# Kernel tuning notes

Hardware: AMD Instinct MI355X
Metric: run time of the kernel (lower is better)

Reference implementation:

```python
import jax, jax.numpy as jnp
import numpy as np

B, N, H = 8, 2048, 256


def setup_inputs() -> dict:
    key = jax.random.key(0)
    ks = jax.random.split(key, 8)
    s = 1.0 / np.sqrt(H)
    return {
        "node": jax.random.normal(ks[0], (B, N, H), dtype=jnp.float32),
        "graph": jax.random.uniform(ks[1], (B, N, N), dtype=jnp.float32),
        "W1": jax.random.normal(ks[2], (H, H), dtype=jnp.float32) * s,
        "b1": jnp.zeros((H,), dtype=jnp.float32),
        "W2": jax.random.normal(ks[3], (H, H), dtype=jnp.float32) * s,
        "b2": jnp.zeros((H,), dtype=jnp.float32),
        "Wout": jax.random.normal(ks[4], (H, 2 * H), dtype=jnp.float32) * (1.0 / np.sqrt(2 * H)),
        "bout": jnp.zeros((H,), dtype=jnp.float32),
    }


def reference(node, graph, W1, b1, W2, b2, Wout, bout):
    # Symmetric normalization D^{-1/2} A D^{-1/2}, batched and vectorized
    # (equivalent to the per-sample diag-mm loop in the original).
    d = jnp.sum(graph, axis=2)                # [B, N] row sums (torch sum(1) on [N,N])
    dinv = d ** -0.5                          # [B, N]
    g = graph * dinv[:, :, None] * dinv[:, None, :]  # [B, N, N]

    # node_info = relu(fc1(g @ node)); fc2(g @ node_info)
    h = jax.nn.relu(jnp.einsum("bnm,bmh->bnh", g, node) @ W1.T + b1)
    h = jax.nn.relu(jnp.einsum("bnm,bmh->bnh", g, h) @ W2.T + b2)

    agg = jnp.concatenate([node, h], axis=2)  # [B, N, 2H]
    return jax.nn.relu(agg @ Wout.T + bout)   # [B, N, H]
```

## Files before the change

### kernel.cpp

```cpp
#include <hip/hip_runtime.h>
#include <stdint.h>

typedef __attribute__((ext_vector_type(4))) float f32x4;
typedef __attribute__((ext_vector_type(8))) short bf16x8;

static __device__ __forceinline__ unsigned short f2bf(float x) {
  unsigned int u = __builtin_bit_cast(unsigned int, x);
  u = (u + 0x7fffu + ((u >> 16) & 1u)) >> 16;
  return (unsigned short)u;
}

#define GLD16(g, l)                                                            \
  __builtin_amdgcn_global_load_lds(                                            \
      (__attribute__((address_space(1))) const void*)(g),                      \
      (__attribute__((address_space(3))) void*)(l), 16, 0, 0)

__global__ __launch_bounds__(256) void rowscale_cvt_k(
    const float* __restrict__ g, float* __restrict__ dinv,
    unsigned short* __restrict__ gb) {
  int row = blockIdx.x * 4 + (threadIdx.x >> 6);
  int lane = threadIdx.x & 63;
  const float* p = g + (long)row * 2048;
  float4 v[8];
  float s = 0.f;
#pragma unroll
  for (int i = 0; i < 8; ++i) {
    v[i] = *(const float4*)(p + (lane + i * 64) * 4);
    s += v[i].x + v[i].y + v[i].z + v[i].w;
  }
#pragma unroll
  for (int off = 32; off; off >>= 1) s += __shfl_xor(s, off, 64);
  float di = rsqrtf(s);
  if (lane == 0) dinv[row] = di;
  unsigned short* q = gb + (long)row * 2048;
#pragma unroll
  for (int i = 0; i < 8; ++i) {
    ushort4 u;
    u.x = f2bf(v[i].x * di); u.y = f2bf(v[i].y * di);
    u.z = f2bf(v[i].z * di); u.w = f2bf(v[i].w * di);
    *(ushort4*)(q + (lane + i * 64) * 4) = u;
  }
}

__global__ __launch_bounds__(256) void cvt_w_k(const float* __restrict__ W1,
                                               const float* __restrict__ W2,
                                               const float* __restrict__ Wout,
                                               unsigned short* __restrict__ wb) {
  int idx = blockIdx.x * 256 + threadIdx.x;
  float v;
  if (idx < 65536) v = W1[idx];
  else if (idx < 131072) v = W2[idx - 65536];
  else v = Wout[idx - 131072];
  wb[idx] = f2bf(v);
}

__global__ __launch_bounds__(256) void prep_node_k(
    const float* __restrict__ node, const float* __restrict__ dinv,
    unsigned short* __restrict__ nodeT, unsigned short* __restrict__ agg) {
  __shared__ unsigned short t[64 * 68];
  int tid = threadIdx.x;
  int m0 = blockIdx.x * 64, h0 = blockIdx.y * 64;
  long b = blockIdx.z;
#pragma unroll
  for (int i = 0; i < 4; ++i) {
    int idx = tid + 256 * i;
    int r = idx >> 4, c4 = idx & 15;
    long m = m0 + r;
    float4 v = *(const float4*)(node + (b * 2048 + m) * 256 + h0 + c4 * 4);
    float di = dinv[b * 2048 + m];
    ushort4 u;
    u.x = f2bf(v.x); u.y = f2bf(v.y); u.z = f2bf(v.z); u.w = f2bf(v.w);
    *(ushort4*)(agg + (b * 2048 + m) * 512 + h0 + c4 * 4) = u;
    t[(c4 * 4 + 0) * 68 + r] = f2bf(v.x * di);
    t[(c4 * 4 + 1) * 68 + r] = f2bf(v.y * di);
    t[(c4 * 4 + 2) * 68 + r] = f2bf(v.z * di);
    t[(c4 * 4 + 3) * 68 + r] = f2bf(v.w * di);
  }
  __syncthreads();
#pragma unroll
  for (int i = 0; i < 4; ++i) {
    int idx = tid + 256 * i;
    int hr = idx >> 4, c4 = idx & 15;
    ushort4 o = *(const ushort4*)(&t[hr * 68 + c4 * 4]);
    *(ushort4*)(nodeT + (b * 256 + h0 + hr) * 2048 + m0 + c4 * 4) = o;
  }
}

template <bool BIAS, bool RELU, bool SCALE, bool TRANS, bool OUTF32>
__global__ __launch_bounds__(256) void gemm32(
    const unsigned short* __restrict__ A, const unsigned short* __restrict__ Bt,
    const float* __restrict__ bias, const float* __restrict__ scale,
    void* __restrict__ Cp, int K, int lda, int ldbt, long bBatch, int ldc) {
  __shared__ char lds[73728];
  char* ldsA = lds;
  char* ldsB = lds + 8192;

  int tid = threadIdx.x;
  int lane = tid & 63;
  int w = tid >> 6;

  int bid = blockIdx.x;
  int tile = ((bid & 7) << 6) + (bid >> 3);
  int row0 = tile * 32;
  int batch = row0 >> 11;
  const unsigned short* Bb = Bt + (long)batch * bBatch;

  int nt = K >> 6;
  f32x4 acc[2][4] = {};

  auto stageA = [&](int kt, int buf) {
    int slot = w * 64 + lane;
    int r = slot >> 3, j = slot & 7;
    int jg = j ^ (r & 7);
    GLD16(A + (long)(row0 + r) * lda + kt * 64 + jg * 8,
          ldsA + buf * 4096 + w * 1024);
  };
  auto stageB = [&](int kt, int buf) {
    char* base = ldsB + buf * 32768;
#pragma unroll
    for (int i = 0; i < 8; ++i) {
      int slot = (w * 8 + i) * 64 + lane;
      int c = slot >> 3, j = slot & 7;
      int jg = j ^ (c & 7);
      GLD16(Bb + (long)c * ldbt + kt * 64 + jg * 8, base + (w * 8 + i) * 1024);
    }
  };
  auto compute = [&](int buf) {
    char* bA = ldsA + buf * 4096;
    char* bB = ldsB + buf * 32768;
    bf16x8 a[2][2], bb[4][2];
#pragma unroll
    for (int m = 0; m < 2; ++m)
#pragma unroll
      for (int kk = 0; kk < 2; ++kk) {
        int row = m * 16 + (lane & 15);
        int off = (row * 128 + kk * 64 + (lane >> 4) * 16) ^ ((row & 7) << 4);
        a[m][kk] = *(const bf16x8*)(bA + off);
      }
#pragma unroll
    for (int n = 0; n < 4; ++n)
#pragma unroll
      for (int kk = 0; kk < 2; ++kk) {
        int col = w * 64 + n * 16 + (lane & 15);
        int off = (col * 128 + kk * 64 + (lane >> 4) * 16) ^ ((col & 7) << 4);
        bb[n][kk] = *(const bf16x8*)(bB + off);
      }
#pragma unroll
    for (int m = 0; m < 2; ++m)
#pragma unroll
      for (int n = 0; n < 4; ++n) {
        acc[m][n] = __builtin_amdgcn_mfma_f32_16x16x32_bf16(a[m][0], bb[n][0],
                                                            acc[m][n], 0, 0, 0);
        acc[m][n] = __builtin_amdgcn_mfma_f32_16x16x32_bf16(a[m][1], bb[n][1],
                                                            acc[m][n], 0, 0, 0);
      }
  };

  stageA(0, 0);
  stageB(0, 0);
  __syncthreads();

  int cur = 0;
  for (int t = 0; t < nt; ++t) {
    int nxt = cur ^ 1;
    if (t + 1 < nt) {
      stageA(t + 1, nxt);
      stageB(t + 1, nxt);
    }
    compute(cur);
    __syncthreads();
    cur = nxt;
  }

  if (TRANS) {
    unsigned short* tb = (unsigned short*)lds;
#pragma unroll
    for (int m = 0; m < 2; ++m)
#pragma unroll
      for (int n = 0; n < 4; ++n) {
        int col = w * 64 + n * 16 + (lane & 15);
        float bv = BIAS ? bias[col] : 0.f;
#pragma unroll
        for (int r = 0; r < 4; ++r) {
          int rl = m * 16 + (lane >> 4) * 4 + r;
          float v = acc[m][n][r];
          if (BIAS) v += bv;
          if (RELU) v = fmaxf(v, 0.f);
          if (SCALE) v *= scale[row0 + rl];
          tb[col * 40 + rl] = f2bf(v);
        }
      }
    __syncthreads();
    unsigned short* C = (unsigned short*)Cp;
    int rin = row0 & 2047;
#pragma unroll
    for (int cc = 0; cc < 4; ++cc) {
      int col = (tid >> 2) + cc * 64;
      int seg = tid & 3;
      bf16x8 u = *(const bf16x8*)(tb + col * 40 + seg * 8);
      *(bf16x8*)(C + ((long)batch * 256 + col) * 2048 + rin + seg * 8) = u;
    }
  } else {
#pragma unroll
    for (int m = 0; m < 2; ++m)
#pragma unroll
      for (int n = 0; n < 4; ++n) {
        int col = w * 64 + n * 16 + (lane & 15);
        float bv = BIAS ? bias[col] : 0.f;
#pragma unroll
        for (int r = 0; r < 4; ++r) {
          long row = row0 + m * 16 + (lane >> 4) * 4 + r;
          float v = acc[m][n][r];
          if (BIAS) v += bv;
          if (RELU) v = fmaxf(v, 0.f);
          if (SCALE) v *= scale[row];
          if (OUTF32) ((float*)Cp)[row * ldc + col] = v;
          else ((unsigned short*)Cp)[row * ldc + col] = f2bf(v);
        }
      }
  }
}

extern "C" void kernel_launch(void* const* d_in, const int* in_sizes, int n_in,
                              void* d_out, int out_size, void* d_ws,
                              size_t ws_size, hipStream_t stream) {
  const float* node = (const float*)d_in[0];
  const float* graph = (const float*)d_in[1];
  const float* W1 = (const float*)d_in[2];
  const float* b1 = (const float*)d_in[3];
  const float* W2 = (const float*)d_in[4];
  const float* b2 = (const float*)d_in[5];
  const float* Wout = (const float*)d_in[6];
  const float* bout = (const float*)d_in[7];
  float* out = (float*)d_out;

  char* p = (char*)d_ws;
  float* dinv = (float*)p;                    p += 16384 * 4;
  unsigned short* wb = (unsigned short*)p;    p += 262144 * 2;
  unsigned short* gb = (unsigned short*)p;    p += 8L * 2048 * 2048 * 2;
  unsigned short* nodeT = (unsigned short*)p; p += 8L * 256 * 2048 * 2;
  unsigned short* bufT = (unsigned short*)p;  p += 8L * 2048 * 256 * 2;
  unsigned short* agg = (unsigned short*)p;   p += 8L * 2048 * 512 * 2;

  rowscale_cvt_k<<<4096, 256, 0, stream>>>(graph, dinv, gb);
  cvt_w_k<<<1024, 256, 0, stream>>>(W1, W2, Wout, wb);
  prep_node_k<<<dim3(32, 4, 8), 256, 0, stream>>>(node, dinv, nodeT, agg);

  gemm32<false, false, false, false, false><<<512, 256, 0, stream>>>(
      gb, nodeT, nullptr, nullptr, bufT, 2048, 2048, 2048, 256L * 2048, 256);
  gemm32<true, true, true, true, false><<<512, 256, 0, stream>>>(
      bufT, wb, b1, dinv, nodeT, 256, 256, 256, 0, 2048);
  gemm32<false, false, false, false, false><<<512, 256, 0, stream>>>(
      gb, nodeT, nullptr, nullptr, bufT, 2048, 2048, 2048, 256L * 2048, 256);
  gemm32<true, true, false, false, false><<<512, 256, 0, stream>>>(
      bufT, wb + 65536, b2, nullptr, agg + 256, 256, 256, 256, 0, 512);
  gemm32<true, true, false, false, true><<<512, 256, 0, stream>>>(
      agg, wb + 131072, bout, nullptr, out, 512, 512, 512, 0, 256);
}
```

Baseline: 314.0 us.

## Enlarge GEMM tile to 128x256 with 8 waves per block

Replaces the 32-row GEMM tile (4 waves, 512 blocks) with a 128-row tile computed by 8 waves arranged 2x4, launching 128 blocks of 512 threads. Each staged B tile (256 columns) is now reused across four times as many A rows, which cuts redundant loads of the node/feature operand from global memory and L2. The cost is only 128 blocks on a 256-CU MI355X, so half the CUs sit idle, plus higher register pressure from the 4x4 accumulator array per wave.

```diff
diff --git a/kernel.cpp b/kernel.cpp
--- a/kernel.cpp
+++ b/kernel.cpp
@@ -87,53 +87,57 @@
 }
 
 template <bool BIAS, bool RELU, bool SCALE, bool TRANS, bool OUTF32>
-__global__ __launch_bounds__(256) void gemm32(
+__global__ __launch_bounds__(512, 1) void gemm128(
     const unsigned short* __restrict__ A, const unsigned short* __restrict__ Bt,
     const float* __restrict__ bias, const float* __restrict__ scale,
     void* __restrict__ Cp, int K, int lda, int ldbt, long bBatch, int ldc) {
-  __shared__ char lds[73728];
+  __shared__ char lds[98304];
   char* ldsA = lds;
-  char* ldsB = lds + 8192;
+  char* ldsB = lds + 32768;
 
   int tid = threadIdx.x;
   int lane = tid & 63;
   int w = tid >> 6;
+  int wm = w >> 2, wn = w & 3;
 
   int bid = blockIdx.x;
-  int tile = ((bid & 7) << 6) + (bid >> 3);
-  int row0 = tile * 32;
-  int batch = row0 >> 11;
+  int tile = ((bid & 7) << 4) + (bid >> 3);
+  long row0 = (long)tile * 128;
+  int batch = (int)(row0 >> 11);
   const unsigned short* Bb = Bt + (long)batch * bBatch;
 
   int nt = K >> 6;
-  f32x4 acc[2][4] = {};
+  f32x4 acc[4][4] = {};
 
   auto stageA = [&](int kt, int buf) {
-    int slot = w * 64 + lane;
-    int r = slot >> 3, j = slot & 7;
-    int jg = j ^ (r & 7);
-    GLD16(A + (long)(row0 + r) * lda + kt * 64 + jg * 8,
-          ldsA + buf * 4096 + w * 1024);
+#pragma unroll
+    for (int i = 0; i < 2; ++i) {
+      int slot = i * 512 + tid;
+      int r = slot >> 3, j = slot & 7;
+      int jg = j ^ (r & 7);
+      GLD16(A + (row0 + r) * lda + kt * 64 + jg * 8,
+            ldsA + buf * 16384 + (i * 8 + w) * 1024);
+    }
   };
   auto stageB = [&](int kt, int buf) {
-    char* base = ldsB + buf * 32768;
-#pragma unroll
-    for (int i = 0; i < 8; ++i) {
-      int slot = (w * 8 + i) * 64 + lane;
+#pragma unroll
+    for (int i = 0; i < 4; ++i) {
+      int slot = i * 512 + tid;
       int c = slot >> 3, j = slot & 7;
       int jg = j ^ (c & 7);
-      GLD16(Bb + (long)c * ldbt + kt * 64 + jg * 8, base + (w * 8 + i) * 1024);
+      GLD16(Bb + (long)c * ldbt + kt * 64 + jg * 8,
+            ldsB + buf * 32768 + (i * 8 + w) * 1024);
     }
   };
   auto compute = [&](int buf) {
-    char* bA = ldsA + buf * 4096;
+    char* bA = ldsA + buf * 16384;
     char* bB = ldsB + buf * 32768;
-    bf16x8 a[2][2], bb[4][2];
-#pragma unroll
-    for (int m = 0; m < 2; ++m)
+    bf16x8 a[4][2], bb[4][2];
+#pragma unroll
+    for (int m = 0; m < 4; ++m)
 #pragma unroll
       for (int kk = 0; kk < 2; ++kk) {
-        int row = m * 16 + (lane & 15);
+        int row = wm * 64 + m * 16 + (lane & 15);
         int off = (row * 128 + kk * 64 + (lane >> 4) * 16) ^ ((row & 7) << 4);
         a[m][kk] = *(const bf16x8*)(bA + off);
       }
@@ -141,12 +145,12 @@
     for (int n = 0; n < 4; ++n)
 #pragma unroll
       for (int kk = 0; kk < 2; ++kk) {
-        int col = w * 64 + n * 16 + (lane & 15);
+        int col = wn * 64 + n * 16 + (lane & 15);
         int off = (col * 128 + kk * 64 + (lane >> 4) * 16) ^ ((col & 7) << 4);
         bb[n][kk] = *(const bf16x8*)(bB + off);
       }
 #pragma unroll
-    for (int m = 0; m < 2; ++m)
+    for (int m = 0; m < 4; ++m)
 #pragma unroll
       for (int n = 0; n < 4; ++n) {
         acc[m][n] = __builtin_amdgcn_mfma_f32_16x16x32_bf16(a[m][0], bb[n][0],
@@ -175,41 +179,41 @@
   if (TRANS) {
     unsigned short* tb = (unsigned short*)lds;
 #pragma unroll
-    for (int m = 0; m < 2; ++m)
+    for (int m = 0; m < 4; ++m)
 #pragma unroll
       for (int n = 0; n < 4; ++n) {
-        int col = w * 64 + n * 16 + (lane & 15);
+        int col = wn * 64 + n * 16 + (lane & 15);
         float bv = BIAS ? bias[col] : 0.f;
 #pragma unroll
         for (int r = 0; r < 4; ++r) {
-          int rl = m * 16 + (lane >> 4) * 4 + r;
+          int rl = wm * 64 + m * 16 + (lane >> 4) * 4 + r;
           float v = acc[m][n][r];
           if (BIAS) v += bv;
           if (RELU) v = fmaxf(v, 0.f);
           if (SCALE) v *= scale[row0 + rl];
-          tb[col * 40 + rl] = f2bf(v);
+          tb[col * 136 + rl] = f2bf(v);
         }
       }
     __syncthreads();
     unsigned short* C = (unsigned short*)Cp;
-    int rin = row0 & 2047;
-#pragma unroll
-    for (int cc = 0; cc < 4; ++cc) {
-      int col = (tid >> 2) + cc * 64;
-      int seg = tid & 3;
-      bf16x8 u = *(const bf16x8*)(tb + col * 40 + seg * 8);
+    int rin = (int)(row0 & 2047);
+#pragma unroll
+    for (int i = 0; i < 8; ++i) {
+      int id = i * 512 + tid;
+      int col = id >> 4, seg = id & 15;
+      bf16x8 u = *(const bf16x8*)(tb + col * 136 + seg * 8);
       *(bf16x8*)(C + ((long)batch * 256 + col) * 2048 + rin + seg * 8) = u;
     }
   } else {
 #pragma unroll
-    for (int m = 0; m < 2; ++m)
+    for (int m = 0; m < 4; ++m)
 #pragma unroll
       for (int n = 0; n < 4; ++n) {
-        int col = w * 64 + n * 16 + (lane & 15);
+        int col = wn * 64 + n * 16 + (lane & 15);
         float bv = BIAS ? bias[col] : 0.f;
 #pragma unroll
         for (int r = 0; r < 4; ++r) {
-          long row = row0 + m * 16 + (lane >> 4) * 4 + r;
+          long row = row0 + wm * 64 + m * 16 + (lane >> 4) * 4 + r;
           float v = acc[m][n][r];
           if (BIAS) v += bv;
           if (RELU) v = fmaxf(v, 0.f);
@@ -246,14 +250,14 @@
   cvt_w_k<<<1024, 256, 0, stream>>>(W1, W2, Wout, wb);
   prep_node_k<<<dim3(32, 4, 8), 256, 0, stream>>>(node, dinv, nodeT, agg);
 
-  gemm32<false, false, false, false, false><<<512, 256, 0, stream>>>(
+  gemm128<false, false, false, false, false><<<128, 512, 0, stream>>>(
       gb, nodeT, nullptr, nullptr, bufT, 2048, 2048, 2048, 256L * 2048, 256);
-  gemm32<true, true, true, true, false><<<512, 256, 0, stream>>>(
+  gemm128<true, true, true, true, false><<<128, 512, 0, stream>>>(
       bufT, wb, b1, dinv, nodeT, 256, 256, 256, 0, 2048);
-  gemm32<false, false, false, false, false><<<512, 256, 0, stream>>>(
+  gemm128<false, false, false, false, false><<<128, 512, 0, stream>>>(
       gb, nodeT, nullptr, nullptr, bufT, 2048, 2048, 2048, 256L * 2048, 256);
-  gemm32<true, true, false, false, false><<<512, 256, 0, stream>>>(
+  gemm128<true, true, false, false, false><<<128, 512, 0, stream>>>(
       bufT, wb + 65536, b2, nullptr, agg + 256, 256, 256, 256, 0, 512);
-  gemm32<true, true, false, false, true><<<512, 256, 0, stream>>>(
+  gemm128<true, true, false, false, true><<<128, 512, 0, stream>>>(
       agg, wb + 131072, bout, nullptr, out, 512, 512, 512, 0, 256);
 }
```

Measured after the change: 320.3 us. 1.02x slower.
